# Optimization experiments

Hardware: AMD Instinct MI355X
Metric: run time of the kernel (lower is better)

The kernel has to match this reference:

```python
import jax, jax.numpy as jnp
import numpy as np

N, E, F_IN, H, L, G = 50000, 800000, 128, 256, 64, 500


def setup_inputs() -> dict:
    key = jax.random.key(0)
    ks = jax.random.split(key, 12)
    s = 0.02
    x = jax.random.normal(ks[0], (N, F_IN), dtype=jnp.float32)
    edge_index = jax.random.randint(ks[1], (2, E), 0, N, dtype=jnp.int64 if jax.config.jax_enable_x64 else jnp.int32)
    batch = jnp.sort(jax.random.randint(ks[2], (N,), 0, G, dtype=jnp.int32))
    return {
        "x": x,
        "edge_index": edge_index,
        "batch": batch,
        "num_graphs": G,
        "W1": jax.random.normal(ks[3], (F_IN, H), dtype=jnp.float32) * s,
        "b1": jnp.zeros((H,), dtype=jnp.float32),
        "W2": jax.random.normal(ks[4], (H, H), dtype=jnp.float32) * s,
        "b2": jnp.zeros((H,), dtype=jnp.float32),
        "Wmu": jax.random.normal(ks[5], (H, L), dtype=jnp.float32) * s,
        "bmu": jnp.zeros((L,), dtype=jnp.float32),
        "Wlv": jax.random.normal(ks[6], (H, L), dtype=jnp.float32) * s,
        "blv": jnp.zeros((L,), dtype=jnp.float32),
    }


def _gcn_norm(edge_index, n_nodes):
    # PyG GCNConv default: add self-loops, symmetric normalization D^-1/2 A_hat D^-1/2
    loop = jnp.arange(n_nodes, dtype=edge_index.dtype)
    src = jnp.concatenate([edge_index[0], loop])
    dst = jnp.concatenate([edge_index[1], loop])
    deg = jax.ops.segment_sum(jnp.ones_like(dst, dtype=jnp.float32), dst, num_segments=n_nodes)
    dinv = jnp.where(deg > 0, jax.lax.rsqrt(deg), 0.0)
    norm = dinv[src] * dinv[dst]  # [E + N]
    return src, dst, norm


def _gcn_conv(h, src, dst, norm, W, b, n_nodes):
    h = h @ W                              # [N, out]
    msg = norm[:, None] * h[src]           # gather + scale: [E+N, out]
    agg = jax.ops.segment_sum(msg, dst, num_segments=n_nodes)  # scatter-add
    return agg + b


def reference(x, edge_index, batch, num_graphs, W1, b1, W2, b2, Wmu, bmu, Wlv, blv):
    n_nodes = x.shape[0]
    src, dst, norm = _gcn_norm(edge_index, n_nodes)
    h = jax.nn.relu(_gcn_conv(x, src, dst, norm, W1, b1, n_nodes))
    h = jax.nn.relu(_gcn_conv(h, src, dst, norm, W2, b2, n_nodes))
    # global_mean_pool over batch ids
    sums = jax.ops.segment_sum(h, batch, num_segments=num_graphs)       # [G, H]
    cnt = jax.ops.segment_sum(jnp.ones((n_nodes,), h.dtype), batch, num_segments=num_graphs)
    h_graph = sums / jnp.maximum(cnt, 1.0)[:, None]
    mu = h_graph @ Wmu + bmu
    logvar = h_graph @ Wlv + blv
    return mu, logvar
```

## Files before the change

kernel.cpp:

```cpp
#include <hip/hip_runtime.h>
#include <hip/hip_fp16.h>

#define N_NODES 50000
#define N_EDGES 800000
#define F_IN_D  128
#define H_DIM   256
#define L_DIM   64
#define G_NUM   500

typedef unsigned int   u32;
typedef unsigned short u16;
typedef unsigned char  u8;
typedef __attribute__((ext_vector_type(8))) short short8;
typedef __attribute__((ext_vector_type(4))) float f32x4;
typedef __attribute__((ext_vector_type(2))) float f32x2;

#define BSHIFT 8
#define NBUCK ((N_NODES + 255) >> BSHIFT)
#define CUR_STRIDE 16
#define BIN_NB 512
#define EPB ((N_EDGES + BIN_NB - 1) / BIN_NB)
#define BUCK_CAP 8192

static __device__ __forceinline__ float bf2f(u16 u) {
    union { u32 i; float f; } x; x.i = ((u32)u) << 16; return x.f;
}
static __device__ __forceinline__ u16 f2bf(float f) {
    union { float f; u32 i; } x; x.f = f;
    u32 r = (x.i + 0x7fffu + ((x.i >> 16) & 1u)) >> 16;
    return (u16)r;
}
static __device__ __forceinline__ float edge_w(u32 e) {
    return __half2float(__ushort_as_half((u16)(e >> 16)));
}

static __device__ __forceinline__ u32 pack4_fp8(u32 a, u32 b) {
    u32 w = __builtin_amdgcn_cvt_pk_fp8_f32(bf2f((u16)(a & 0xffff)),
                                            bf2f((u16)(a >> 16)), 0, false);
    w = __builtin_amdgcn_cvt_pk_fp8_f32(bf2f((u16)(b & 0xffff)),
                                        bf2f((u16)(b >> 16)), w, true);
    return w;
}

static __device__ __forceinline__ u32 bswz_idx(int n, int k, int plane, int KS) {
    int n0g = n >> 6, nt = (n >> 4) & 3, lr = n & 15;
    int k0i = k >> 5, ks = k & 31, lq = ks >> 3, j = ks & 7;
    return ((u32)((((n0g * KS + k0i) * 2 + plane) * 4 + nt) * 64 + lq * 16 + lr)) * 8 + j;
}

#define NXQ (N_NODES * F_IN_D / 4)
#define NW1 (F_IN_D * H_DIM)
#define NW2 (H_DIM * H_DIM)
#define NB_SCAN  ((N_NODES + 255) / 256)
#define NB_CONV  ((NXQ + NW1 + NW2 + 255) / 256)

__global__ void prep_kernel(const int* __restrict__ src, const int* __restrict__ dst,
                            const int* __restrict__ batch, int* __restrict__ goff,
                            const float* __restrict__ x, u8* __restrict__ xq,
                            const float* __restrict__ W1, u16* __restrict__ w1swz,
                            const float* __restrict__ W2, u16* __restrict__ w2swz,
                            int* __restrict__ bcur, u32* __restrict__ binrec) {
    int b = blockIdx.x;
    if (b < BIN_NB) {
        __shared__ int lhist[NBUCK];
        __shared__ int lbase[NBUCK];
        int t = threadIdx.x;
        int e0 = b * EPB;
        int e1 = e0 + EPB; if (e1 > N_EDGES) e1 = N_EDGES;
        for (int i = t; i < NBUCK; i += 256) lhist[i] = 0;
        __syncthreads();
        for (int e = e0 + t; e < e1; e += 256)
            atomicAdd(&lhist[dst[e] >> BSHIFT], 1);
        __syncthreads();
        for (int i = t; i < NBUCK; i += 256) {
            int c = lhist[i];
            lbase[i] = i * BUCK_CAP + (c ? atomicAdd(&bcur[i * CUR_STRIDE], c) : 0);
            lhist[i] = 0;
        }
        __syncthreads();
        for (int e = e0 + t; e < e1; e += 256) {
            int d = dst[e], s = src[e];
            int bkt = d >> BSHIFT;
            int rank = atomicAdd(&lhist[bkt], 1);
            binrec[(size_t)lbase[bkt] + rank] = (u32)s | ((u32)(d & 255) << 16);
        }
    } else if (b < BIN_NB + NB_SCAN) {
        int i = (b - BIN_NB) * 256 + threadIdx.x;
        if (i >= N_NODES) return;
        int v = batch[i];
        if (i == 0) {
            for (int g = 0; g <= v; ++g) goff[g] = 0;
        } else {
            int p = batch[i - 1];
            for (int g = p + 1; g <= v; ++g) goff[g] = i;
        }
        if (i == N_NODES - 1) {
            for (int g = v + 1; g <= G_NUM; ++g) goff[g] = N_NODES;
        }
    } else {
        int i = (b - BIN_NB - NB_SCAN) * 256 + threadIdx.x;
        if (i < NXQ) {
            float4 v = *(const float4*)&x[(size_t)i * 4];
            u32 w = __builtin_amdgcn_cvt_pk_fp8_f32(v.x, v.y, 0, false);
            w = __builtin_amdgcn_cvt_pk_fp8_f32(v.z, v.w, w, true);
            *(u32*)&xq[(size_t)i * 4] = w;
        } else if (i < NXQ + NW1) {
            int idx = i - NXQ;
            int k = idx >> 8, n = idx & 255;
            float w = W1[idx];
            u16 h = f2bf(w);
            w1swz[bswz_idx(n, k, 0, F_IN_D / 32)] = h;
            w1swz[bswz_idx(n, k, 1, F_IN_D / 32)] = f2bf(w - bf2f(h));
        } else if (i < NXQ + NW1 + NW2) {
            int idx = i - NXQ - NW1;
            int k = idx >> 8, n = idx & 255;
            float w = W2[idx];
            u16 h = f2bf(w);
            w2swz[bswz_idx(n, k, 0, H_DIM / 32)] = h;
            w2swz[bswz_idx(n, k, 1, H_DIM / 32)] = f2bf(w - bf2f(h));
        }
    }
}

__global__ __launch_bounds__(256)
void cnt_scan_kernel(const int* __restrict__ bcur, const u32* __restrict__ binrec,
                     int* __restrict__ excl, int* __restrict__ partials,
                     float* __restrict__ dinv) {
    __shared__ int lh[256];
    __shared__ int sm[256];
    int b = blockIdx.x;
    int t = threadIdx.x;
    lh[t] = 0;
    __syncthreads();
    int s0 = b * BUCK_CAP;
    int s1 = s0 + bcur[b * CUR_STRIDE];
    for (int p = s0 + t; p < s1; p += 256)
        atomicAdd(&lh[(binrec[p] >> 16) & 255], 1);
    __syncthreads();
    int i = (b << BSHIFT) + t;
    int v = lh[t];
    sm[t] = v; __syncthreads();
    for (int off = 1; off < 256; off <<= 1) {
        int x = (t >= off) ? sm[t - off] : 0;
        __syncthreads();
        sm[t] += x;
        __syncthreads();
    }
    if (i < N_NODES) {
        excl[i] = sm[t] - v;
        dinv[i] = 1.0f / sqrtf((float)(v + 1));
    }
    if (t == 255) partials[b] = sm[255];
}

__global__ void scan_final_kernel(const int* __restrict__ excl, const int* __restrict__ partials,
                                  int* __restrict__ out, int n, int nb) {
    __shared__ int sm[256];
    int t = threadIdx.x;
    int v = (t < nb) ? partials[t] : 0;
    sm[t] = v; __syncthreads();
    for (int off = 1; off < 256; off <<= 1) {
        int x = (t >= off) ? sm[t - off] : 0;
        __syncthreads();
        sm[t] += x;
        __syncthreads();
    }
    int pre = (blockIdx.x > 0) ? sm[blockIdx.x - 1] : 0;
    int i = blockIdx.x * 256 + t;
    if (i < n) out[i] = excl[i] + pre;
    if (blockIdx.x == (unsigned)(nb - 1) && t == 0) out[n] = sm[nb - 1];
}

__global__ __launch_bounds__(256)
void place2_kernel(const int* __restrict__ rp, const int* __restrict__ bcur,
                   const u32* __restrict__ binrec, const float* __restrict__ dinv,
                   u32* __restrict__ csr) {
    __shared__ int ncur[256];
    int b = blockIdx.x;
    int t = threadIdx.x;
    int n0 = b << BSHIFT;
    int n1 = n0 + 256; if (n1 > N_NODES) n1 = N_NODES;
    if (n0 + t < n1) ncur[t] = rp[n0 + t];
    __syncthreads();
    int s0 = b * BUCK_CAP;
    int s1 = s0 + bcur[b * CUR_STRIDE];
    for (int p = s0 + t; p < s1; p += 256) {
        u32 r = binrec[p];
        int s = (int)(r & 0xffff);
        int pos = atomicAdd(&ncur[(r >> 16) & 255], 1);
        u32 w = (u32)__half_as_ushort(__float2half(dinv[s]));
        csr[pos] = (u32)s | (w << 16);
    }
}

__global__ __launch_bounds__(256)
void agg128_fp8_kernel(const u8* __restrict__ In, const float* __restrict__ dinv,
                       const int* __restrict__ rp, const u32* __restrict__ csr,
                       u16* __restrict__ Out) {
    int node = blockIdx.x * 4 + (threadIdx.x >> 6);
    int lane = threadIdx.x & 63;
    if (node >= N_NODES) return;
    int c = lane * 2;
    float di = dinv[node];
    int r0 = rp[node], r1 = rp[node + 1];
    u32 sv = *(const u16*)&In[(size_t)node * 128 + c];
    f32x2 s = __builtin_amdgcn_cvt_pk_f32_fp8(sv, false);
    float a0 = di * s.x;
    float a1 = di * s.y;
    int j = r0;
    for (; j + 8 <= r1; j += 8) {
        u32 e[8];
        u32 v[8];
#pragma unroll
        for (int q = 0; q < 8; ++q) e[q] = csr[j + q];
#pragma unroll
        for (int q = 0; q < 8; ++q) v[q] = *(const u16*)&In[(size_t)(e[q] & 0xffff) * 128 + c];
#pragma unroll
        for (int q = 0; q < 8; ++q) {
            float w = edge_w(e[q]);
            f32x2 p = __builtin_amdgcn_cvt_pk_f32_fp8(v[q], false);
            a0 = fmaf(w, p.x, a0);
            a1 = fmaf(w, p.y, a1);
        }
    }
    for (; j + 4 <= r1; j += 4) {
        u32 e[4];
        u32 v[4];
#pragma unroll
        for (int q = 0; q < 4; ++q) e[q] = csr[j + q];
#pragma unroll
        for (int q = 0; q < 4; ++q) v[q] = *(const u16*)&In[(size_t)(e[q] & 0xffff) * 128 + c];
#pragma unroll
        for (int q = 0; q < 4; ++q) {
            float w = edge_w(e[q]);
            f32x2 p = __builtin_amdgcn_cvt_pk_f32_fp8(v[q], false);
            a0 = fmaf(w, p.x, a0);
            a1 = fmaf(w, p.y, a1);
        }
    }
    for (; j < r1; ++j) {
        u32 e = csr[j];
        u32 v = *(const u16*)&In[(size_t)(e & 0xffff) * 128 + c];
        float w = edge_w(e);
        f32x2 p = __builtin_amdgcn_cvt_pk_f32_fp8(v, false);
        a0 = fmaf(w, p.x, a0);
        a1 = fmaf(w, p.y, a1);
    }
    u32 o = ((u32)f2bf(di * a1) << 16) | (u32)f2bf(di * a0);
    *(u32*)&Out[(size_t)node * 128 + c] = o;
}

__global__ __launch_bounds__(256)
void agg256_fp8_kernel(const u8* __restrict__ In, const float* __restrict__ dinv,
                       const int* __restrict__ rp, const u32* __restrict__ csr,
                       u16* __restrict__ Out) {
    int node = blockIdx.x * 4 + (threadIdx.x >> 6);
    int lane = threadIdx.x & 63;
    if (node >= N_NODES) return;
    int c = lane * 4;
    float di = dinv[node];
    int r0 = rp[node], r1 = rp[node + 1];
    u32 sv = *(const u32*)&In[(size_t)node * 256 + c];
    f32x2 s01 = __builtin_amdgcn_cvt_pk_f32_fp8(sv, false);
    f32x2 s23 = __builtin_amdgcn_cvt_pk_f32_fp8(sv, true);
    float a0 = di * s01.x;
    float a1 = di * s01.y;
    float a2 = di * s23.x;
    float a3 = di * s23.y;
    int j = r0;
    for (; j + 8 <= r1; j += 8) {
        u32 e[8];
        u32 v[8];
#pragma unroll
        for (int q = 0; q < 8; ++q) e[q] = csr[j + q];
#pragma unroll
        for (int q = 0; q < 8; ++q) v[q] = *(const u32*)&In[(size_t)(e[q] & 0xffff) * 256 + c];
#pragma unroll
        for (int q = 0; q < 8; ++q) {
            float w = edge_w(e[q]);
            f32x2 p0 = __builtin_amdgcn_cvt_pk_f32_fp8(v[q], false);
            f32x2 p1 = __builtin_amdgcn_cvt_pk_f32_fp8(v[q], true);
            a0 = fmaf(w, p0.x, a0);
            a1 = fmaf(w, p0.y, a1);
            a2 = fmaf(w, p1.x, a2);
            a3 = fmaf(w, p1.y, a3);
        }
    }
    for (; j + 4 <= r1; j += 4) {
        u32 e[4];
        u32 v[4];
#pragma unroll
        for (int q = 0; q < 4; ++q) e[q] = csr[j + q];
#pragma unroll
        for (int q = 0; q < 4; ++q) v[q] = *(const u32*)&In[(size_t)(e[q] & 0xffff) * 256 + c];
#pragma unroll
        for (int q = 0; q < 4; ++q) {
            float w = edge_w(e[q]);
            f32x2 p0 = __builtin_amdgcn_cvt_pk_f32_fp8(v[q], false);
            f32x2 p1 = __builtin_amdgcn_cvt_pk_f32_fp8(v[q], true);
            a0 = fmaf(w, p0.x, a0);
            a1 = fmaf(w, p0.y, a1);
            a2 = fmaf(w, p1.x, a2);
            a3 = fmaf(w, p1.y, a3);
        }
    }
    for (; j < r1; ++j) {
        u32 e = csr[j];
        u32 v = *(const u32*)&In[(size_t)(e & 0xffff) * 256 + c];
        float w = edge_w(e);
        f32x2 p0 = __builtin_amdgcn_cvt_pk_f32_fp8(v, false);
        f32x2 p1 = __builtin_amdgcn_cvt_pk_f32_fp8(v, true);
        a0 = fmaf(w, p0.x, a0);
        a1 = fmaf(w, p0.y, a1);
        a2 = fmaf(w, p1.x, a2);
        a3 = fmaf(w, p1.y, a3);
    }
    uint2 o;
    o.x = ((u32)f2bf(di * a1) << 16) | (u32)f2bf(di * a0);
    o.y = ((u32)f2bf(di * a3) << 16) | (u32)f2bf(di * a2);
    *(uint2*)&Out[(size_t)node * 256 + c] = o;
}

template<int K>
__global__ __launch_bounds__(256, 3)
void gemm1_kernel(const u16* __restrict__ A, const short8* __restrict__ Bswz,
                  const float* __restrict__ bias, u8* __restrict__ Out, int M) {
    const int KS = K / 32;
    __shared__ u16 cst[64][264];
    int tid  = threadIdx.x;
    int wave = tid >> 6, lane = tid & 63;
    int m0 = blockIdx.x * 64;
    int n0 = wave * 64;
    int lr = lane & 15;
    int lk = (lane >> 4) * 8;

    f32x4 acc[4][4];
#pragma unroll
    for (int i = 0; i < 4; ++i)
#pragma unroll
        for (int j = 0; j < 4; ++j) acc[i][j] = {0.f, 0.f, 0.f, 0.f};

    for (int k0i = 0; k0i < KS; ++k0i) {
        int k0 = k0i * 32;
        short8 a[4], bh[4], bl[4];
#pragma unroll
        for (int mt = 0; mt < 4; ++mt) {
            int m = m0 + mt * 16 + lr;
            if (m > M - 1) m = M - 1;
            a[mt] = *(const short8*)&A[(size_t)m * K + k0 + lk];
        }
        const short8* bp = Bswz + ((size_t)(wave * KS + k0i) * 8) * 64 + lane;
#pragma unroll
        for (int nt = 0; nt < 4; ++nt) {
            bh[nt] = bp[(size_t)nt * 64];
            bl[nt] = bp[(size_t)(4 + nt) * 64];
        }
#pragma unroll
        for (int mt = 0; mt < 4; ++mt)
#pragma unroll
            for (int nt = 0; nt < 4; ++nt) {
                acc[mt][nt] = __builtin_amdgcn_mfma_f32_16x16x32_bf16(a[mt], bh[nt], acc[mt][nt], 0, 0, 0);
                acc[mt][nt] = __builtin_amdgcn_mfma_f32_16x16x32_bf16(a[mt], bl[nt], acc[mt][nt], 0, 0, 0);
            }
    }

#pragma unroll
    for (int mt = 0; mt < 4; ++mt)
#pragma unroll
        for (int nt = 0; nt < 4; ++nt) {
            int col = n0 + nt * 16 + lr;
            float b = bias[col];
#pragma unroll
            for (int r = 0; r < 4; ++r) {
                int row = mt * 16 + (lane >> 4) * 4 + r;
                cst[row][col] = f2bf(fmaxf(acc[mt][nt][r] + b, 0.f));
            }
        }
    __syncthreads();
#pragma unroll
    for (int p = 0; p < 8; ++p) {
        int row = p * 8 + (tid >> 5);
        int c16 = (tid & 31) * 8;
        int m = m0 + row;
        if (m < M) {
            uint4 v = *(const uint4*)&cst[row][c16];
            uint2 o = make_uint2(pack4_fp8(v.x, v.y), pack4_fp8(v.z, v.w));
            *(uint2*)&Out[(size_t)m * 256 + c16] = o;
        }
    }
}

__global__ __launch_bounds__(256, 3)
void gemm2_pool_kernel(const u16* __restrict__ A, const short8* __restrict__ Bswz,
                       const float* __restrict__ bias, const int* __restrict__ batch,
                       float* __restrict__ pooled, int M) {
    const int K = H_DIM, KS = K / 32;
    __shared__ u16 cst[64][264];
    __shared__ int batch_s[64];
    int tid  = threadIdx.x;
    int wave = tid >> 6, lane = tid & 63;
    int m0 = blockIdx.x * 64;
    int n0 = wave * 64;
    int lr = lane & 15;
    int lk = (lane >> 4) * 8;

    f32x4 acc[4][4];
#pragma unroll
    for (int i = 0; i < 4; ++i)
#pragma unroll
        for (int j = 0; j < 4; ++j) acc[i][j] = {0.f, 0.f, 0.f, 0.f};

    for (int k0i = 0; k0i < KS; ++k0i) {
        int k0 = k0i * 32;
        short8 a[4], bh[4], bl[4];
#pragma unroll
        for (int mt = 0; mt < 4; ++mt) {
            int m = m0 + mt * 16 + lr;
            if (m > M - 1) m = M - 1;
            a[mt] = *(const short8*)&A[(size_t)m * K + k0 + lk];
        }
        const short8* bp = Bswz + ((size_t)(wave * KS + k0i) * 8) * 64 + lane;
#pragma unroll
        for (int nt = 0; nt < 4; ++nt) {
            bh[nt] = bp[(size_t)nt * 64];
            bl[nt] = bp[(size_t)(4 + nt) * 64];
        }
#pragma unroll
        for (int mt = 0; mt < 4; ++mt)
#pragma unroll
            for (int nt = 0; nt < 4; ++nt) {
                acc[mt][nt] = __builtin_amdgcn_mfma_f32_16x16x32_bf16(a[mt], bh[nt], acc[mt][nt], 0, 0, 0);
                acc[mt][nt] = __builtin_amdgcn_mfma_f32_16x16x32_bf16(a[mt], bl[nt], acc[mt][nt], 0, 0, 0);
            }
    }

    if (tid < 64) {
        int m = m0 + tid;
        batch_s[tid] = (m < M) ? batch[m] : -1;
    }
#pragma unroll
    for (int mt = 0; mt < 4; ++mt)
#pragma unroll
        for (int nt = 0; nt < 4; ++nt) {
            int col = n0 + nt * 16 + lr;
            float b = bias[col];
#pragma unroll
            for (int r = 0; r < 4; ++r) {
                int row = mt * 16 + (lane >> 4) * 4 + r;
                cst[row][col] = f2bf(fmaxf(acc[mt][nt][r] + b, 0.f));
            }
        }
    __syncthreads();

    int rows = M - m0; if (rows > 64) rows = 64;
    float s = 0.f;
    int gp = batch_s[0];
    for (int r = 0; r < rows; ++r) {
        int g = batch_s[r];
        if (g != gp) {
            atomicAdd(&pooled[(size_t)gp * H_DIM + tid], s);
            s = 0.f;
            gp = g;
        }
        s += bf2f(cst[r][tid]);
    }
    atomicAdd(&pooled[(size_t)gp * H_DIM + tid], s);
}

__global__ void head_kernel(const float* __restrict__ pooled, const int* __restrict__ goff,
                            const float* __restrict__ Wmu, const float* __restrict__ bmu,
                            const float* __restrict__ Wlv, const float* __restrict__ blv,
                            float* __restrict__ out) {
    __shared__ float hg[H_DIM];
    int g = blockIdx.x, l = threadIdx.x;
    float inv = 1.0f / fmaxf((float)(goff[g + 1] - goff[g]), 1.0f);
    for (int k = l; k < H_DIM; k += 64) hg[k] = pooled[(size_t)g * H_DIM + k] * inv;
    __syncthreads();
    float mu = bmu[l], lv = blv[l];
    for (int k = 0; k < H_DIM; ++k) {
        float h = hg[k];
        mu = fmaf(h, Wmu[k * L_DIM + l], mu);
        lv = fmaf(h, Wlv[k * L_DIM + l], lv);
    }
    out[(size_t)g * L_DIM + l] = mu;
    out[(size_t)G_NUM * L_DIM + (size_t)g * L_DIM + l] = lv;
}

extern "C" void kernel_launch(void* const* d_in, const int* in_sizes, int n_in,
                              void* d_out, int out_size, void* d_ws, size_t ws_size,
                              hipStream_t stream) {
    const float* x     = (const float*)d_in[0];
    const int*   ei    = (const int*)  d_in[1];
    const int*   batch = (const int*)  d_in[2];
    const float* W1  = (const float*)d_in[4];
    const float* b1  = (const float*)d_in[5];
    const float* W2  = (const float*)d_in[6];
    const float* b2  = (const float*)d_in[7];
    const float* Wmu = (const float*)d_in[8];
    const float* bmu = (const float*)d_in[9];
    const float* Wlv = (const float*)d_in[10];
    const float* blv = (const float*)d_in[11];
    const int* src = ei;
    const int* dst = ei + N_EDGES;

    char* ws = (char*)d_ws;
    size_t off = 0;
    auto alloc = [&](size_t bytes) -> void* {
        void* p = ws + off;
        off += (bytes + 255) & ~(size_t)255;
        return p;
    };
    float* pooled   = (float*)alloc((size_t)G_NUM * H_DIM * 4);
    int*   bcur     = (int*)alloc((size_t)NBUCK * CUR_STRIDE * 4);
    float* dinv     = (float*)alloc((size_t)N_NODES * 4);
    int*   row_ptr  = (int*)alloc((size_t)(N_NODES + 1) * 4);
    u32*   csr      = (u32*)alloc((size_t)N_EDGES * 4);
    u32*   binrec   = (u32*)alloc((size_t)NBUCK * BUCK_CAP * 4);
    int*   excl     = (int*)alloc((size_t)N_NODES * 4);
    int*   partials = (int*)alloc(256 * 4);
    int*   goff     = (int*)alloc((size_t)(G_NUM + 1) * 4);
    u8*    xq    = (u8*)alloc((size_t)N_NODES * F_IN_D);
    u16*   Xa    = (u16*)alloc((size_t)N_NODES * F_IN_D * 2);
    u8*    H8    = (u8*)alloc((size_t)N_NODES * H_DIM);
    u16*   Ha    = (u16*)alloc((size_t)N_NODES * H_DIM * 2);
    u16*   w1swz = (u16*)alloc((size_t)2 * F_IN_D * H_DIM * 2);
    u16*   w2swz = (u16*)alloc((size_t)2 * H_DIM * H_DIM * 2);
    (void)ws_size; (void)n_in; (void)in_sizes; (void)out_size;

    const int GEMM_NB = (N_NODES + 63) / 64;
    size_t zero_bytes = (size_t)((char*)(bcur + NBUCK * CUR_STRIDE) - (char*)pooled);

    hipMemsetAsync(pooled, 0, zero_bytes, stream);
    prep_kernel<<<BIN_NB + NB_SCAN + NB_CONV, 256, 0, stream>>>(
        src, dst, batch, goff, x, xq, W1, w1swz, W2, w2swz, bcur, binrec);
    cnt_scan_kernel<<<NBUCK, 256, 0, stream>>>(bcur, binrec, excl, partials, dinv);
    scan_final_kernel<<<NB_SCAN, 256, 0, stream>>>(excl, partials, row_ptr, N_NODES, NB_SCAN);
    place2_kernel<<<NBUCK, 256, 0, stream>>>(row_ptr, bcur, binrec, dinv, csr);

    agg128_fp8_kernel<<<(N_NODES + 3) / 4, 256, 0, stream>>>(xq, dinv, row_ptr, csr, Xa);
    gemm1_kernel<F_IN_D><<<GEMM_NB, 256, 0, stream>>>(Xa, (const short8*)w1swz, b1, H8, N_NODES);
    agg256_fp8_kernel<<<(N_NODES + 3) / 4, 256, 0, stream>>>(H8, dinv, row_ptr, csr, Ha);
    gemm2_pool_kernel<<<GEMM_NB, 256, 0, stream>>>(Ha, (const short8*)w2swz, b2, batch, pooled, N_NODES);

    head_kernel<<<G_NUM, 64, 0, stream>>>(pooled, goff, Wmu, bmu, Wlv, blv, (float*)d_out);
}
```

Before: 255.7 us.

## Fuse neighbor aggregation into GEMM kernels and merge scan into placement

Each aggregation kernel is folded into its following MFMA GEMM kernel: a 64-row block first gathers and aggregates its own nodes into shared memory as bf16, then runs the GEMM from shared memory. This removes the bf16 intermediate buffers Xa and Ha and their global write/read round trips, plus two kernel launches. The final scan is also merged into the CSR placement kernel, saving another launch. The trade-off is that the gather phase now runs with one block per 64 nodes and launch bounds sized for the GEMM, so it has less latency hiding, and the gather and MFMA phases no longer overlap across separate kernels.

```diff
diff --git a/kernel.cpp b/kernel.cpp
--- a/kernel.cpp
+++ b/kernel.cpp
@@ -153,11 +153,16 @@
     if (t == 255) partials[b] = sm[255];
 }
 
-__global__ void scan_final_kernel(const int* __restrict__ excl, const int* __restrict__ partials,
-                                  int* __restrict__ out, int n, int nb) {
+__global__ __launch_bounds__(256)
+void place2_kernel(const int* __restrict__ excl, const int* __restrict__ partials,
+                   const int* __restrict__ bcur, const u32* __restrict__ binrec,
+                   const float* __restrict__ dinv,
+                   int* __restrict__ rp, u32* __restrict__ csr) {
     __shared__ int sm[256];
+    __shared__ int ncur[256];
+    int b = blockIdx.x;
     int t = threadIdx.x;
-    int v = (t < nb) ? partials[t] : 0;
+    int v = (t < NBUCK) ? partials[t] : 0;
     sm[t] = v; __syncthreads();
     for (int off = 1; off < 256; off <<= 1) {
         int x = (t >= off) ? sm[t - off] : 0;
@@ -165,22 +170,15 @@
         sm[t] += x;
         __syncthreads();
     }
-    int pre = (blockIdx.x > 0) ? sm[blockIdx.x - 1] : 0;
-    int i = blockIdx.x * 256 + t;
-    if (i < n) out[i] = excl[i] + pre;
-    if (blockIdx.x == (unsigned)(nb - 1) && t == 0) out[n] = sm[nb - 1];
-}
-
-__global__ __launch_bounds__(256)
-void place2_kernel(const int* __restrict__ rp, const int* __restrict__ bcur,
-                   const u32* __restrict__ binrec, const float* __restrict__ dinv,
-                   u32* __restrict__ csr) {
-    __shared__ int ncur[256];
-    int b = blockIdx.x;
-    int t = threadIdx.x;
+    int pre = (b > 0) ? sm[b - 1] : 0;
     int n0 = b << BSHIFT;
-    int n1 = n0 + 256; if (n1 > N_NODES) n1 = N_NODES;
-    if (n0 + t < n1) ncur[t] = rp[n0 + t];
+    int i = n0 + t;
+    if (i < N_NODES) {
+        int base = excl[i] + pre;
+        rp[i] = base;
+        ncur[t] = base;
+    }
+    if (b == NBUCK - 1 && t == 0) rp[N_NODES] = sm[NBUCK - 1];
     __syncthreads();
     int s0 = b * BUCK_CAP;
     int s1 = s0 + bcur[b * CUR_STRIDE];
@@ -193,147 +191,77 @@
     }
 }
 
-__global__ __launch_bounds__(256)
-void agg128_fp8_kernel(const u8* __restrict__ In, const float* __restrict__ dinv,
-                       const int* __restrict__ rp, const u32* __restrict__ csr,
-                       u16* __restrict__ Out) {
-    int node = blockIdx.x * 4 + (threadIdx.x >> 6);
-    int lane = threadIdx.x & 63;
-    if (node >= N_NODES) return;
-    int c = lane * 2;
-    float di = dinv[node];
-    int r0 = rp[node], r1 = rp[node + 1];
-    u32 sv = *(const u16*)&In[(size_t)node * 128 + c];
-    f32x2 s = __builtin_amdgcn_cvt_pk_f32_fp8(sv, false);
-    float a0 = di * s.x;
-    float a1 = di * s.y;
-    int j = r0;
-    for (; j + 8 <= r1; j += 8) {
-        u32 e[8];
-        u32 v[8];
-#pragma unroll
-        for (int q = 0; q < 8; ++q) e[q] = csr[j + q];
-#pragma unroll
-        for (int q = 0; q < 8; ++q) v[q] = *(const u16*)&In[(size_t)(e[q] & 0xffff) * 128 + c];
-#pragma unroll
-        for (int q = 0; q < 8; ++q) {
-            float w = edge_w(e[q]);
-            f32x2 p = __builtin_amdgcn_cvt_pk_f32_fp8(v[q], false);
-            a0 = fmaf(w, p.x, a0);
-            a1 = fmaf(w, p.y, a1);
-        }
-    }
-    for (; j + 4 <= r1; j += 4) {
-        u32 e[4];
-        u32 v[4];
-#pragma unroll
-        for (int q = 0; q < 4; ++q) e[q] = csr[j + q];
-#pragma unroll
-        for (int q = 0; q < 4; ++q) v[q] = *(const u16*)&In[(size_t)(e[q] & 0xffff) * 128 + c];
-#pragma unroll
-        for (int q = 0; q < 4; ++q) {
-            float w = edge_w(e[q]);
-            f32x2 p = __builtin_amdgcn_cvt_pk_f32_fp8(v[q], false);
-            a0 = fmaf(w, p.x, a0);
-            a1 = fmaf(w, p.y, a1);
-        }
-    }
-    for (; j < r1; ++j) {
-        u32 e = csr[j];
-        u32 v = *(const u16*)&In[(size_t)(e & 0xffff) * 128 + c];
-        float w = edge_w(e);
-        f32x2 p = __builtin_amdgcn_cvt_pk_f32_fp8(v, false);
-        a0 = fmaf(w, p.x, a0);
-        a1 = fmaf(w, p.y, a1);
-    }
-    u32 o = ((u32)f2bf(di * a1) << 16) | (u32)f2bf(di * a0);
-    *(u32*)&Out[(size_t)node * 128 + c] = o;
-}
-
-__global__ __launch_bounds__(256)
-void agg256_fp8_kernel(const u8* __restrict__ In, const float* __restrict__ dinv,
-                       const int* __restrict__ rp, const u32* __restrict__ csr,
-                       u16* __restrict__ Out) {
-    int node = blockIdx.x * 4 + (threadIdx.x >> 6);
-    int lane = threadIdx.x & 63;
-    if (node >= N_NODES) return;
-    int c = lane * 4;
-    float di = dinv[node];
-    int r0 = rp[node], r1 = rp[node + 1];
-    u32 sv = *(const u32*)&In[(size_t)node * 256 + c];
-    f32x2 s01 = __builtin_amdgcn_cvt_pk_f32_fp8(sv, false);
-    f32x2 s23 = __builtin_amdgcn_cvt_pk_f32_fp8(sv, true);
-    float a0 = di * s01.x;
-    float a1 = di * s01.y;
-    float a2 = di * s23.x;
-    float a3 = di * s23.y;
-    int j = r0;
-    for (; j + 8 <= r1; j += 8) {
-        u32 e[8];
-        u32 v[8];
-#pragma unroll
-        for (int q = 0; q < 8; ++q) e[q] = csr[j + q];
-#pragma unroll
-        for (int q = 0; q < 8; ++q) v[q] = *(const u32*)&In[(size_t)(e[q] & 0xffff) * 256 + c];
-#pragma unroll
-        for (int q = 0; q < 8; ++q) {
-            float w = edge_w(e[q]);
-            f32x2 p0 = __builtin_amdgcn_cvt_pk_f32_fp8(v[q], false);
-            f32x2 p1 = __builtin_amdgcn_cvt_pk_f32_fp8(v[q], true);
-            a0 = fmaf(w, p0.x, a0);
-            a1 = fmaf(w, p0.y, a1);
-            a2 = fmaf(w, p1.x, a2);
-            a3 = fmaf(w, p1.y, a3);
-        }
-    }
-    for (; j + 4 <= r1; j += 4) {
-        u32 e[4];
-        u32 v[4];
-#pragma unroll
-        for (int q = 0; q < 4; ++q) e[q] = csr[j + q];
-#pragma unroll
-        for (int q = 0; q < 4; ++q) v[q] = *(const u32*)&In[(size_t)(e[q] & 0xffff) * 256 + c];
-#pragma unroll
-        for (int q = 0; q < 4; ++q) {
-            float w = edge_w(e[q]);
-            f32x2 p0 = __builtin_amdgcn_cvt_pk_f32_fp8(v[q], false);
-            f32x2 p1 = __builtin_amdgcn_cvt_pk_f32_fp8(v[q], true);
-            a0 = fmaf(w, p0.x, a0);
-            a1 = fmaf(w, p0.y, a1);
-            a2 = fmaf(w, p1.x, a2);
-            a3 = fmaf(w, p1.y, a3);
-        }
-    }
-    for (; j < r1; ++j) {
-        u32 e = csr[j];
-        u32 v = *(const u32*)&In[(size_t)(e & 0xffff) * 256 + c];
-        float w = edge_w(e);
-        f32x2 p0 = __builtin_amdgcn_cvt_pk_f32_fp8(v, false);
-        f32x2 p1 = __builtin_amdgcn_cvt_pk_f32_fp8(v, true);
-        a0 = fmaf(w, p0.x, a0);
-        a1 = fmaf(w, p0.y, a1);
-        a2 = fmaf(w, p1.x, a2);
-        a3 = fmaf(w, p1.y, a3);
-    }
-    uint2 o;
-    o.x = ((u32)f2bf(di * a1) << 16) | (u32)f2bf(di * a0);
-    o.y = ((u32)f2bf(di * a3) << 16) | (u32)f2bf(di * a2);
-    *(uint2*)&Out[(size_t)node * 256 + c] = o;
-}
-
-template<int K>
+#define A1_STRIDE 136
 __global__ __launch_bounds__(256, 3)
-void gemm1_kernel(const u16* __restrict__ A, const short8* __restrict__ Bswz,
-                  const float* __restrict__ bias, u8* __restrict__ Out, int M) {
-    const int KS = K / 32;
-    __shared__ u16 cst[64][264];
+void agg_gemm1_kernel(const u8* __restrict__ In, const float* __restrict__ dinv,
+                      const int* __restrict__ rp, const u32* __restrict__ csr,
+                      const short8* __restrict__ Bswz, const float* __restrict__ bias,
+                      u8* __restrict__ Out, int M) {
+    const int K = F_IN_D, KS = K / 32;
+    __shared__ u16 smem[64 * 264];
     int tid  = threadIdx.x;
     int wave = tid >> 6, lane = tid & 63;
     int m0 = blockIdx.x * 64;
+
+    {
+        int c = lane * 2;
+        for (int nn = 0; nn < 16; ++nn) {
+            int node = m0 + wave * 16 + nn;
+            float a0 = 0.f, a1 = 0.f;
+            if (node < M) {
+                float di = dinv[node];
+                int r0 = rp[node], r1 = rp[node + 1];
+                u32 sv = *(const u16*)&In[(size_t)node * 128 + c];
+                f32x2 s = __builtin_amdgcn_cvt_pk_f32_fp8(sv, false);
+                a0 = di * s.x;
+                a1 = di * s.y;
+                int j = r0;
+                for (; j + 8 <= r1; j += 8) {
+                    u32 e[8], v[8];
+#pragma unroll
+                    for (int q = 0; q < 8; ++q) e[q] = csr[j + q];
+#pragma unroll
+                    for (int q = 0; q < 8; ++q) v[q] = *(const u16*)&In[(size_t)(e[q] & 0xffff) * 128 + c];
+#pragma unroll
+                    for (int q = 0; q < 8; ++q) {
+                        float w = edge_w(e[q]);
+                        f32x2 p = __builtin_amdgcn_cvt_pk_f32_fp8(v[q], false);
+                        a0 = fmaf(w, p.x, a0);
+                        a1 = fmaf(w, p.y, a1);
+                    }
+                }
+                for (; j + 4 <= r1; j += 4) {
+                    u32 e[4], v[4];
+#pragma unroll
+                    for (int q = 0; q < 4; ++q) e[q] = csr[j + q];
+#pragma unroll
+                    for (int q = 0; q < 4; ++q) v[q] = *(const u16*)&In[(size_t)(e[q] & 0xffff) * 128 + c];
+#pragma unroll
+                    for (int q = 0; q < 4; ++q) {
+                        float w = edge_w(e[q]);
+                        f32x2 p = __builtin_amdgcn_cvt_pk_f32_fp8(v[q], false);
+                        a0 = fmaf(w, p.x, a0);
+                        a1 = fmaf(w, p.y, a1);
+                    }
+                }
+                for (; j < r1; ++j) {
+                    u32 e = csr[j];
+                    u32 v = *(const u16*)&In[(size_t)(e & 0xffff) * 128 + c];
+                    float w = edge_w(e);
+                    f32x2 p = __builtin_amdgcn_cvt_pk_f32_fp8(v, false);
+                    a0 = fmaf(w, p.x, a0);
+                    a1 = fmaf(w, p.y, a1);
+                }
+                a0 *= di; a1 *= di;
+            }
+            *(u32*)&smem[(wave * 16 + nn) * A1_STRIDE + c] = ((u32)f2bf(a1) << 16) | (u32)f2bf(a0);
+        }
+    }
+    __syncthreads();
+
     int n0 = wave * 64;
     int lr = lane & 15;
     int lk = (lane >> 4) * 8;
-
     f32x4 acc[4][4];
 #pragma unroll
     for (int i = 0; i < 4; ++i)
@@ -344,11 +272,8 @@
         int k0 = k0i * 32;
         short8 a[4], bh[4], bl[4];
 #pragma unroll
-        for (int mt = 0; mt < 4; ++mt) {
-            int m = m0 + mt * 16 + lr;
-            if (m > M - 1) m = M - 1;
-            a[mt] = *(const short8*)&A[(size_t)m * K + k0 + lk];
-        }
+        for (int mt = 0; mt < 4; ++mt)
+            a[mt] = *(const short8*)&smem[(mt * 16 + lr) * A1_STRIDE + k0 + lk];
         const short8* bp = Bswz + ((size_t)(wave * KS + k0i) * 8) * 64 + lane;
 #pragma unroll
         for (int nt = 0; nt < 4; ++nt) {
@@ -363,6 +288,7 @@
                 acc[mt][nt] = __builtin_amdgcn_mfma_f32_16x16x32_bf16(a[mt], bl[nt], acc[mt][nt], 0, 0, 0);
             }
     }
+    __syncthreads();
 
 #pragma unroll
     for (int mt = 0; mt < 4; ++mt)
@@ -373,7 +299,7 @@
 #pragma unroll
             for (int r = 0; r < 4; ++r) {
                 int row = mt * 16 + (lane >> 4) * 4 + r;
-                cst[row][col] = f2bf(fmaxf(acc[mt][nt][r] + b, 0.f));
+                smem[row * 264 + col] = f2bf(fmaxf(acc[mt][nt][r] + b, 0.f));
             }
         }
     __syncthreads();
@@ -383,7 +309,7 @@
         int c16 = (tid & 31) * 8;
         int m = m0 + row;
         if (m < M) {
-            uint4 v = *(const uint4*)&cst[row][c16];
+            uint4 v = *(const uint4*)&smem[row * 264 + c16];
             uint2 o = make_uint2(pack4_fp8(v.x, v.y), pack4_fp8(v.z, v.w));
             *(uint2*)&Out[(size_t)m * 256 + c16] = o;
         }
@@ -391,19 +317,95 @@
 }
 
 __global__ __launch_bounds__(256, 3)
-void gemm2_pool_kernel(const u16* __restrict__ A, const short8* __restrict__ Bswz,
-                       const float* __restrict__ bias, const int* __restrict__ batch,
-                       float* __restrict__ pooled, int M) {
+void agg_gemm2_pool_kernel(const u8* __restrict__ In, const float* __restrict__ dinv,
+                           const int* __restrict__ rp, const u32* __restrict__ csr,
+                           const short8* __restrict__ Bswz, const float* __restrict__ bias,
+                           const int* __restrict__ batch, float* __restrict__ pooled, int M) {
     const int K = H_DIM, KS = K / 32;
-    __shared__ u16 cst[64][264];
+    __shared__ u16 smem[64 * 264];
     __shared__ int batch_s[64];
     int tid  = threadIdx.x;
     int wave = tid >> 6, lane = tid & 63;
     int m0 = blockIdx.x * 64;
+
+    {
+        int c = lane * 4;
+        for (int nn = 0; nn < 16; ++nn) {
+            int node = m0 + wave * 16 + nn;
+            float a0 = 0.f, a1 = 0.f, a2 = 0.f, a3 = 0.f;
+            if (node < M) {
+                float di = dinv[node];
+                int r0 = rp[node], r1 = rp[node + 1];
+                u32 sv = *(const u32*)&In[(size_t)node * 256 + c];
+                f32x2 s01 = __builtin_amdgcn_cvt_pk_f32_fp8(sv, false);
+                f32x2 s23 = __builtin_amdgcn_cvt_pk_f32_fp8(sv, true);
+                a0 = di * s01.x;
+                a1 = di * s01.y;
+                a2 = di * s23.x;
+                a3 = di * s23.y;
+                int j = r0;
+                for (; j + 8 <= r1; j += 8) {
+                    u32 e[8], v[8];
+#pragma unroll
+                    for (int q = 0; q < 8; ++q) e[q] = csr[j + q];
+#pragma unroll
+                    for (int q = 0; q < 8; ++q) v[q] = *(const u32*)&In[(size_t)(e[q] & 0xffff) * 256 + c];
+#pragma unroll
+                    for (int q = 0; q < 8; ++q) {
+                        float w = edge_w(e[q]);
+                        f32x2 p0 = __builtin_amdgcn_cvt_pk_f32_fp8(v[q], false);
+                        f32x2 p1 = __builtin_amdgcn_cvt_pk_f32_fp8(v[q], true);
+                        a0 = fmaf(w, p0.x, a0);
+                        a1 = fmaf(w, p0.y, a1);
+                        a2 = fmaf(w, p1.x, a2);
+                        a3 = fmaf(w, p1.y, a3);
+                    }
+                }
+                for (; j + 4 <= r1; j += 4) {
+                    u32 e[4], v[4];
+#pragma unroll
+                    for (int q = 0; q < 4; ++q) e[q] = csr[j + q];
+#pragma unroll
+                    for (int q = 0; q < 4; ++q) v[q] = *(const u32*)&In[(size_t)(e[q] & 0xffff) * 256 + c];
+#pragma unroll
+                    for (int q = 0; q < 4; ++q) {
+                        float w = edge_w(e[q]);
+                        f32x2 p0 = __builtin_amdgcn_cvt_pk_f32_fp8(v[q], false);
+                        f32x2 p1 = __builtin_amdgcn_cvt_pk_f32_fp8(v[q], true);
+                        a0 = fmaf(w, p0.x, a0);
+                        a1 = fmaf(w, p0.y, a1);
+                        a2 = fmaf(w, p1.x, a2);
+                        a3 = fmaf(w, p1.y, a3);
+                    }
+                }
+                for (; j < r1; ++j) {
+                    u32 e = csr[j];
+                    u32 v = *(const u32*)&In[(size_t)(e & 0xffff) * 256 + c];
+                    float w = edge_w(e);
+                    f32x2 p0 = __builtin_amdgcn_cvt_pk_f32_fp8(v, false);
+                    f32x2 p1 = __builtin_amdgcn_cvt_pk_f32_fp8(v, true);
+                    a0 = fmaf(w, p0.x, a0);
+                    a1 = fmaf(w, p0.y, a1);
+                    a2 = fmaf(w, p1.x, a2);
+                    a3 = fmaf(w, p1.y, a3);
+                }
+                a0 *= di; a1 *= di; a2 *= di; a3 *= di;
+            }
+            uint2 o;
+            o.x = ((u32)f2bf(a1) << 16) | (u32)f2bf(a0);
+            o.y = ((u32)f2bf(a3) << 16) | (u32)f2bf(a2);
+            *(uint2*)&smem[(wave * 16 + nn) * 264 + c] = o;
+        }
+    }
+    if (tid < 64) {
+        int m = m0 + tid;
+        batch_s[tid] = (m < M) ? batch[m] : -1;
+    }
+    __syncthreads();
+
     int n0 = wave * 64;
     int lr = lane & 15;
     int lk = (lane >> 4) * 8;
-
     f32x4 acc[4][4];
 #pragma unroll
     for (int i = 0; i < 4; ++i)
@@ -414,11 +416,8 @@
         int k0 = k0i * 32;
         short8 a[4], bh[4], bl[4];
 #pragma unroll
-        for (int mt = 0; mt < 4; ++mt) {
-            int m = m0 + mt * 16 + lr;
-            if (m > M - 1) m = M - 1;
-            a[mt] = *(const short8*)&A[(size_t)m * K + k0 + lk];
-        }
+        for (int mt = 0; mt < 4; ++mt)
+            a[mt] = *(const short8*)&smem[(mt * 16 + lr) * 264 + k0 + lk];
         const short8* bp = Bswz + ((size_t)(wave * KS + k0i) * 8) * 64 + lane;
 #pragma unroll
         for (int nt = 0; nt < 4; ++nt) {
@@ -433,11 +432,8 @@
                 acc[mt][nt] = __builtin_amdgcn_mfma_f32_16x16x32_bf16(a[mt], bl[nt], acc[mt][nt], 0, 0, 0);
             }
     }
-
-    if (tid < 64) {
-        int m = m0 + tid;
-        batch_s[tid] = (m < M) ? batch[m] : -1;
-    }
+    __syncthreads();
+
 #pragma unroll
     for (int mt = 0; mt < 4; ++mt)
 #pragma unroll
@@ -447,7 +443,7 @@
 #pragma unroll
             for (int r = 0; r < 4; ++r) {
                 int row = mt * 16 + (lane >> 4) * 4 + r;
-                cst[row][col] = f2bf(fmaxf(acc[mt][nt][r] + b, 0.f));
+                smem[row * 264 + col] = f2bf(fmaxf(acc[mt][nt][r] + b, 0.f));
             }
         }
     __syncthreads();
@@ -462,7 +458,7 @@
             s = 0.f;
             gp = g;
         }
-        s += bf2f(cst[r][tid]);
+        s += bf2f(smem[r * 264 + tid]);
     }
     atomicAdd(&pooled[(size_t)gp * H_DIM + tid], s);
 }
@@ -520,9 +516,7 @@
     int*   partials = (int*)alloc(256 * 4);
     int*   goff     = (int*)alloc((size_t)(G_NUM + 1) * 4);
     u8*    xq    = (u8*)alloc((size_t)N_NODES * F_IN_D);
-    u16*   Xa    = (u16*)alloc((size_t)N_NODES * F_IN_D * 2);
     u8*    H8    = (u8*)alloc((size_t)N_NODES * H_DIM);
-    u16*   Ha    = (u16*)alloc((size_t)N_NODES * H_DIM * 2);
     u16*   w1swz = (u16*)alloc((size_t)2 * F_IN_D * H_DIM * 2);
     u16*   w2swz = (u16*)alloc((size_t)2 * H_DIM * H_DIM * 2);
     (void)ws_size; (void)n_in; (void)in_sizes; (void)out_size;
@@ -534,13 +528,12 @@
     prep_kernel<<<BIN_NB + NB_SCAN + NB_CONV, 256, 0, stream>>>(
         src, dst, batch, goff, x, xq, W1, w1swz, W2, w2swz, bcur, binrec);
     cnt_scan_kernel<<<NBUCK, 256, 0, stream>>>(bcur, binrec, excl, partials, dinv);
-    scan_final_kernel<<<NB_SCAN, 256, 0, stream>>>(excl, partials, row_ptr, N_NODES, NB_SCAN);
-    place2_kernel<<<NBUCK, 256, 0, stream>>>(row_ptr, bcur, binrec, dinv, csr);
-
-    agg128_fp8_kernel<<<(N_NODES + 3) / 4, 256, 0, stream>>>(xq, dinv, row_ptr, csr, Xa);
-    gemm1_kernel<F_IN_D><<<GEMM_NB, 256, 0, stream>>>(Xa, (const short8*)w1swz, b1, H8, N_NODES);
-    agg256_fp8_kernel<<<(N_NODES + 3) / 4, 256, 0, stream>>>(H8, dinv, row_ptr, csr, Ha);
-    gemm2_pool_kernel<<<GEMM_NB, 256, 0, stream>>>(Ha, (const short8*)w2swz, b2, batch, pooled, N_NODES);
+    place2_kernel<<<NBUCK, 256, 0, stream>>>(excl, partials, bcur, binrec, dinv, row_ptr, csr);
+
+    agg_gemm1_kernel<<<GEMM_NB, 256, 0, stream>>>(
+        xq, dinv, row_ptr, csr, (const short8*)w1swz, b1, H8, N_NODES);
+    agg_gemm2_pool_kernel<<<GEMM_NB, 256, 0, stream>>>(
+        H8, dinv, row_ptr, csr, (const short8*)w2swz, b2, batch, pooled, N_NODES);
 
     head_kernel<<<G_NUM, 64, 0, stream>>>(pooled, goff, Wmu, bmu, Wlv, blv, (float*)d_out);
 }
```

New measurement: 332.6 us. 30.1% more time.
